# Optimization experiments

Hardware: AMD Instinct MI355X
Metric: run time of the kernel (lower is better)

Reference implementation:

```python
import jax, jax.numpy as jnp
import numpy as np

B, S, D, H, E = 2, 2048, 1024, 16, 8
DH = D // H
CAP_FACTOR = 1.2


def setup_inputs() -> dict:
    key = jax.random.key(0)
    ks = jax.random.split(key, 14)
    s = 0.02
    return {
        "embed": jax.random.normal(ks[0], (B, S, D), jnp.float32),
        "Wq": jax.random.normal(ks[1], (H, DH, D), jnp.float32) * s,
        "bq": jnp.zeros((H, DH), jnp.float32),
        "Wk": jax.random.normal(ks[2], (H, DH, D), jnp.float32) * s,
        "bk": jnp.zeros((H, DH), jnp.float32),
        "Wv": jax.random.normal(ks[3], (H, DH, D), jnp.float32) * s,
        "bv": jnp.zeros((H, DH), jnp.float32),
        "We": jax.random.normal(ks[4], (E, D, D), jnp.float32) * s,
        "be": jnp.zeros((E, D), jnp.float32),
        "Wsw": jax.random.normal(ks[5], (E, D), jnp.float32) * s,
        "bsw": jnp.zeros((E,), jnp.float32),
        "gamma": jnp.ones((D,), jnp.float32),
        "beta": jnp.zeros((D,), jnp.float32),
    }


def _forward(embed, Wq, bq, Wk, bk, Wv, bv, We, be, Wsw, bsw, gamma, beta):
    b, s, d = embed.shape
    h, e = Wq.shape[0], We.shape[0]
    # --- multi-head attention (all heads batched via einsum) ---
    q = jnp.einsum('bsd,hed->bhse', embed, Wq) + bq[None, :, None, :]
    k = jnp.einsum('bsd,hed->bhse', embed, Wk) + bk[None, :, None, :]
    v = jnp.einsum('bsd,hed->bhse', embed, Wv) + bv[None, :, None, :]
    att = jnp.einsum('bhse,bhte->bhst', q, k)  # [b,h,s,s]
    tril = jnp.tril(jnp.ones((s, s), bool))
    # faithful: upper triangle zeroed (NOT -inf), scale by sqrt(embedding_dim)
    att = jnp.where(tril, att, 0.0) / jnp.sqrt(jnp.float32(d))
    att = jax.nn.softmax(att, axis=-1)
    out = jnp.einsum('bhst,bhte->bhse', att, v)
    hiddens = out.transpose(0, 2, 1, 3).reshape(b, s, d)
    # --- SwitchLinear: top-1 token-choice routing with capacity drop ---
    x = hiddens.reshape(-1, d)  # [N, d]
    n = b * s
    capacity = int(CAP_FACTOR * n / e)
    logits = x @ Wsw.T + bsw
    probs = jax.nn.softmax(logits, axis=-1)
    route_probs = jnp.max(probs, axis=-1)
    routes = jnp.argmax(probs, axis=-1)
    onehot = jax.nn.one_hot(routes, e, dtype=jnp.int32)
    pos = jnp.cumsum(onehot, axis=0) - 1  # position within chosen expert
    pos = jnp.take_along_axis(pos, routes[:, None], axis=1)[:, 0]
    kept = pos < capacity
    slot = jnp.where(kept, routes * capacity + pos, e * capacity)  # overflow row
    dispatch = jnp.zeros((e * capacity + 1, d), x.dtype).at[slot].set(x)
    expert_in = dispatch[: e * capacity].reshape(e, capacity, d)
    expert_out = jnp.einsum('ecd,efd->ecf', expert_in, We) + be[:, None, :]
    expert_flat = jnp.concatenate(
        [expert_out.reshape(e * capacity, d), jnp.zeros((1, d), x.dtype)], 0)
    gathered = expert_flat[slot]
    y = jnp.where(kept[:, None], gathered, x)  # dropped tokens pass through
    y = (y * route_probs[:, None]).reshape(b, s, d)
    # --- residual + LayerNorm ---
    x2 = y + embed
    mean = jnp.mean(x2, axis=-1, keepdims=True)
    var = jnp.var(x2, axis=-1, keepdims=True)
    return (x2 - mean) / jnp.sqrt(var + 1e-5) * gamma + beta


def reference(embed, Wq, bq, Wk, bk, Wv, bv, We, be, Wsw, bsw, gamma, beta):
    return _forward(embed, Wq, bq, Wk, bk, Wv, bv, We, be, Wsw, bsw, gamma, beta)
```

## Files before the change

### kernel.cpp

```cpp
#include <hip/hip_runtime.h>

constexpr int B = 2, S = 2048, D = 1024, H = 16, E = 8, DH = 64;
constexpr int N = B * S;
constexpr int CAP = 614;
constexpr int ECAP = 640;
constexpr float INV_SQRT_D = 0.03125f;
constexpr int ATTN_LDS = 133120;

typedef __bf16 bf16x8 __attribute__((ext_vector_type(8)));
typedef float f32x4 __attribute__((ext_vector_type(4)));

__device__ __forceinline__ ushort f2bf(float x) {
  __bf16 h = (__bf16)x;
  return __builtin_bit_cast(unsigned short, h);
}
__device__ __forceinline__ float bf2f(ushort u) {
  __bf16 h = __builtin_bit_cast(__bf16, u);
  return (float)h;
}
__device__ __forceinline__ void gld16(const void* g, void* l) {
  __builtin_amdgcn_global_load_lds(
      (const __attribute__((address_space(1))) unsigned int*)g,
      (__attribute__((address_space(3))) unsigned int*)l, 16, 0, 0);
}

__global__ __launch_bounds__(256) void cvt_pair(const float* __restrict__ in,
                                                ushort* __restrict__ out)
{
  const long long idx4 = (long long)blockIdx.x * 256 + threadIdx.x;
  const float4 xv = ((const float4*)in)[idx4];
  const long long row = idx4 >> 8;
  const int col = (int)((idx4 & 255) << 2);
  float xs[4] = {xv.x, xv.y, xv.z, xv.w};
  ushort4 hi, lo;
  ushort* hp = (ushort*)&hi; ushort* lp = (ushort*)&lo;
  #pragma unroll
  for (int c = 0; c < 4; ++c) {
    ushort h = f2bf(xs[c]);
    hp[c] = h;
    lp[c] = f2bf(xs[c] - bf2f(h));
  }
  *(ushort4*)&out[row * 2048 + col] = hi;
  *(ushort4*)&out[row * 2048 + 1024 + col] = lo;
}

__global__ __launch_bounds__(256) void cvt_plain(const float* __restrict__ in,
                                                 ushort* __restrict__ out)
{
  const long long idx4 = (long long)blockIdx.x * 256 + threadIdx.x;
  const float4 xv = ((const float4*)in)[idx4];
  ushort4 o;
  o.x = f2bf(xv.x); o.y = f2bf(xv.y); o.z = f2bf(xv.z); o.w = f2bf(xv.w);
  *(ushort4*)&out[idx4 * 4] = o;
}

template <bool TRIPLE, int EPI>
__global__ __launch_bounds__(256) void mfma_gemm(
    const ushort* __restrict__ A, const ushort* __restrict__ W,
    const float* __restrict__ b0, const float* __restrict__ b1,
    const float* __restrict__ b2, float* __restrict__ C,
    ushort* __restrict__ pairout,
    long long strideA, long long strideW, long long strideC,
    long long biasStride, int biasSel)
{
  constexpr int KA = TRIPLE ? 2048 : 1024;
  constexpr int KW = TRIPLE ? 2048 : 1024;
  constexpr int NSTEP = TRIPLE ? 48 : 16;
  const int z = blockIdx.z;
  A += (long long)z * strideA;
  W += (long long)z * strideW;
  C += (long long)z * strideC;
  const float* bp = biasSel ? (z == 0 ? b0 : (z == 1 ? b1 : b2))
                            : b0 + (long long)z * biasStride;

  __shared__ char smem[32768] __attribute__((aligned(128)));
  const int tid = threadIdx.x;
  const int lane = tid & 63;
  const int lrow = lane & 15;
  const int lk = lane >> 4;
  const int wv = tid >> 6;
  const int rAc = (wv >> 1) * 64;
  const int rBc = (wv & 1) * 64;
  const int bm0 = blockIdx.y * 128;
  const int bn0 = blockIdx.x * 128;
  const int srow = tid >> 3;
  const int su = tid & 7;

  f32x4 acc[4][4] = {};

  for (int step = 0; step < NSTEP; ++step) {
    const int k0 = step * 64;
    int srcA, srcB;
    if (TRIPLE) {
      srcA = (k0 < 2048) ? k0 : k0 - 2048;
      srcB = (k0 < 1024) ? k0 : k0 - 1024;
    } else { srcA = k0; srcB = k0; }
    __syncthreads();
    #pragma unroll
    for (int i = 0; i < 4; ++i) {
      const int row = i * 32 + srow;
      const int u = su ^ (row & 7);
      gld16(A + (long long)(bm0 + row) * KA + srcA + u * 8,
            smem + i * 4096 + wv * 1024);
      gld16(W + (long long)(bn0 + row) * KW + srcB + u * 8,
            smem + 16384 + i * 4096 + wv * 1024);
    }
    asm volatile("s_waitcnt vmcnt(0)" ::: "memory");
    __syncthreads();
    #pragma unroll
    for (int h = 0; h < 2; ++h) {
      bf16x8 af[4], bfr[4];
      #pragma unroll
      for (int i = 0; i < 4; ++i) {
        const int row = rAc + i * 16 + lrow;
        const int u = (h * 4 + lk) ^ (row & 7);
        af[i] = *(const bf16x8*)(smem + row * 128 + u * 16);
      }
      #pragma unroll
      for (int j = 0; j < 4; ++j) {
        const int row = rBc + j * 16 + lrow;
        const int u = (h * 4 + lk) ^ (row & 7);
        bfr[j] = *(const bf16x8*)(smem + 16384 + row * 128 + u * 16);
      }
      #pragma unroll
      for (int i = 0; i < 4; ++i)
        #pragma unroll
        for (int j = 0; j < 4; ++j)
          acc[i][j] = __builtin_amdgcn_mfma_f32_16x16x32_bf16(
              af[i], bfr[j], acc[i][j], 0, 0, 0);
    }
  }
  const int rg = (lane >> 4) * 4;
  #pragma unroll
  for (int j = 0; j < 4; ++j) {
    const int col = bn0 + rBc + j * 16 + (lane & 15);
    const float bj = bp[col];
    #pragma unroll
    for (int i = 0; i < 4; ++i) {
      const int rbase = bm0 + rAc + i * 16 + rg;
      if constexpr (EPI == 0) {
        #pragma unroll
        for (int r = 0; r < 4; ++r)
          C[(long long)(rbase + r) * 1024 + col] = acc[i][j][r] + bj;
      } else {
        const int hh = col >> 6, e = col & 63;
        const int b = rbase >> 11;
        if (z < 2) {
          const int sbase = rbase & 2047;
          ushort* dst = pairout + (long long)z * 8388608 +
                        ((long long)(b * 16 + hh) * 2048 + sbase) * 128 + e;
          #pragma unroll
          for (int r = 0; r < 4; ++r) {
            float val = acc[i][j][r] + bj;
            ushort vh = f2bf(val);
            dst[r * 128] = vh;
            dst[r * 128 + 64] = f2bf(val - bf2f(vh));
          }
        } else {
          const int tb = rbase & 2047;
          ushort4 hi4, lo4;
          ushort* hp = (ushort*)&hi4; ushort* lp = (ushort*)&lo4;
          #pragma unroll
          for (int r = 0; r < 4; ++r) {
            float val = acc[i][j][r] + bj;
            ushort vh = f2bf(val);
            hp[r] = vh;
            lp[r] = f2bf(val - bf2f(vh));
          }
          ushort* vdst = pairout + 2ll * 8388608 +
                         (long long)(b * 16 + hh) * 262144 +
                         (long long)e * 2048 + tb;
          *(ushort4*)vdst = hi4;
          *(ushort4*)(vdst + 131072) = lo4;
        }
      }
    }
  }
}

__global__ __launch_bounds__(256) void suffix_kernel(const ushort* __restrict__ vtp,
                                                     float* __restrict__ vsuf)
{
  const int R = blockIdx.x;
  const int bh = R >> 6, e = R & 63;
  const ushort* hi = vtp + (long long)bh * 262144 + (long long)e * 2048;
  const ushort* lo = hi + 131072;
  const int tid = threadIdx.x;
  ushort4 h0 = *(const ushort4*)(hi + tid * 8);
  ushort4 h1 = *(const ushort4*)(hi + tid * 8 + 4);
  ushort4 l0 = *(const ushort4*)(lo + tid * 8);
  ushort4 l1 = *(const ushort4*)(lo + tid * 8 + 4);
  float v[8];
  v[0] = bf2f(h0.x) + bf2f(l0.x); v[1] = bf2f(h0.y) + bf2f(l0.y);
  v[2] = bf2f(h0.z) + bf2f(l0.z); v[3] = bf2f(h0.w) + bf2f(l0.w);
  v[4] = bf2f(h1.x) + bf2f(l1.x); v[5] = bf2f(h1.y) + bf2f(l1.y);
  v[6] = bf2f(h1.z) + bf2f(l1.z); v[7] = bf2f(h1.w) + bf2f(l1.w);
  float s = 0.f;
  #pragma unroll
  for (int x = 0; x < 8; ++x) s += v[x];
  __shared__ float ss[256];
  ss[tid] = s;
  __syncthreads();
  for (int off = 1; off < 256; off <<= 1) {
    float t = (tid + off < 256) ? ss[tid + off] : 0.f;
    __syncthreads();
    ss[tid] += t;
    __syncthreads();
  }
  float acc = (tid < 255) ? ss[tid + 1] : 0.f;
  float out[8];
  for (int x = 7; x >= 0; --x) { acc += v[x]; out[x] = acc; }
  #pragma unroll
  for (int x = 0; x < 8; ++x)
    vsuf[(long long)R * 2048 + tid * 8 + x] = out[x];
}

__device__ __forceinline__ void attn_stage_kv(
    const ushort* kbase, const ushort* vbase, int t0,
    char* kdst, char* vdst, int tid, int wv)
{
  #pragma unroll
  for (int i = 0; i < 2; ++i) {
    const int L = i * 512 + tid;
    const int row = L >> 4, u = L & 15;
    gld16(kbase + (long long)(t0 + row) * 128 + ((u ^ (row & 15)) * 8),
          kdst + i * 8192 + wv * 1024);
  }
  #pragma unroll
  for (int i = 0; i < 2; ++i) {
    const int L = i * 512 + tid;
    const int sec = L >> 9, vr = (L >> 3) & 63, u = L & 7;
    gld16(vbase + (long long)sec * 131072 + (long long)vr * 2048 + t0 +
              ((u ^ (vr & 7)) * 8),
          vdst + i * 8192 + wv * 1024);
  }
}

__global__ __launch_bounds__(512) void attn_mfma(
    const ushort* __restrict__ qp, const ushort* __restrict__ kp,
    const ushort* __restrict__ vtp, const float* __restrict__ vsuf,
    float* __restrict__ hid)
{
  extern __shared__ char smem[];
  const int bh = blockIdx.y;
  const int qi = (int)(gridDim.x - 1 - blockIdx.x);
  const int sB0 = qi * 128;
  const int tid = threadIdx.x;
  const int lane = tid & 63;
  const int wv = tid >> 6;
  const int g = lane >> 4, c = lane & 15;

  ushort* qs = (ushort*)smem;
  char* kbuf0 = smem + 32768;
  char* kbuf1 = smem + 49152;
  char* vbuf0 = smem + 65536;
  char* vbuf1 = smem + 81920;
  float* wl = (float*)(smem + 98304);

  const ushort* qbase = qp + (long long)bh * 2048 * 128;
  const ushort* kbase = kp + (long long)bh * 2048 * 128;
  const ushort* vbase = vtp + (long long)bh * 262144;

  #pragma unroll
  for (int i = 0; i < 4; ++i) {
    const int L = i * 512 + tid;
    const int row = L >> 4, u = L & 15;
    gld16(qbase + (long long)(sB0 + row) * 128 + ((u ^ (row & 15)) * 8),
          smem + i * 8192 + wv * 1024);
  }
  char* kcur = kbuf0; char* knext = kbuf1;
  char* vcur = vbuf0; char* vnext = vbuf1;
  attn_stage_kv(kbase, vbase, 0, kcur, vcur, tid, wv);

  f32x4 oacc[4] = {};
  float l_acc[4] = {};
  const int nt = 2 * qi + 2;
  const int qrow = wv * 16 + c;

  for (int t = 0; t < nt; ++t) {
    const int t0 = t * 64;
    if (t + 1 < nt) {
      attn_stage_kv(kbase, vbase, t0 + 64, knext, vnext, tid, wv);
      asm volatile("s_waitcnt vmcnt(4)" ::: "memory");
    } else {
      asm volatile("s_waitcnt vmcnt(0)" ::: "memory");
    }
    __builtin_amdgcn_s_barrier();

    const ushort* ks = (const ushort*)kcur;
    const ushort* vt = (const ushort*)vcur;

    f32x4 acc[4] = {};
    #pragma unroll
    for (int h = 0; h < 2; ++h) {
      bf16x8 qh = *(const bf16x8*)(qs + qrow * 128 + (((h * 4 + g) ^ (qrow & 15)) * 8));
      bf16x8 ql = *(const bf16x8*)(qs + qrow * 128 + (((8 + h * 4 + g) ^ (qrow & 15)) * 8));
      #pragma unroll
      for (int j = 0; j < 4; ++j) {
        const int krow = j * 16 + c;
        bf16x8 kh = *(const bf16x8*)(ks + krow * 128 + (((h * 4 + g) ^ (krow & 15)) * 8));
        bf16x8 kl = *(const bf16x8*)(ks + krow * 128 + (((8 + h * 4 + g) ^ (krow & 15)) * 8));
        acc[j] = __builtin_amdgcn_mfma_f32_16x16x32_bf16(qh, kh, acc[j], 0, 0, 0);
        acc[j] = __builtin_amdgcn_mfma_f32_16x16x32_bf16(ql, kh, acc[j], 0, 0, 0);
        acc[j] = __builtin_amdgcn_mfma_f32_16x16x32_bf16(qh, kl, acc[j], 0, 0, 0);
      }
    }

    float prt[4] = {0.f, 0.f, 0.f, 0.f};
    #pragma unroll
    for (int j = 0; j < 4; ++j) {
      #pragma unroll
      for (int r = 0; r < 4; ++r) {
        const int sg = sB0 + wv * 16 + 4 * g + r;
        const int tg = t0 + j * 16 + c;
        const float w = (tg <= sg) ? __expf(acc[j][r] * INV_SQRT_D) : 0.f;
        wl[(wv * 16 + 4 * g + r) * 68 + j * 16 + c] = w;
        prt[r] += w;
      }
    }
    #pragma unroll
    for (int off = 1; off < 16; off <<= 1)
      #pragma unroll
      for (int r = 0; r < 4; ++r) prt[r] += __shfl_xor(prt[r], off);
    #pragma unroll
    for (int r = 0; r < 4; ++r) l_acc[r] += prt[r];

    asm volatile("s_waitcnt lgkmcnt(0)" ::: "memory");
    __builtin_amdgcn_s_barrier();

    #pragma unroll
    for (int h = 0; h < 2; ++h) {
      const int wrow = wv * 16 + c;
      const float4 w0 = *(const float4*)&wl[wrow * 68 + h * 32 + g * 8];
      const float4 w1 = *(const float4*)&wl[wrow * 68 + h * 32 + g * 8 + 4];
      const float wf[8] = {w0.x, w0.y, w0.z, w0.w, w1.x, w1.y, w1.z, w1.w};
      bf16x8 wh, wlo;
      #pragma unroll
      for (int x = 0; x < 8; ++x) {
        __bf16 hh = (__bf16)wf[x];
        wh[x] = hh;
        wlo[x] = (__bf16)(wf[x] - (float)hh);
      }
      #pragma unroll
      for (int j = 0; j < 4; ++j) {
        const int vrow = j * 16 + c;
        bf16x8 vh = *(const bf16x8*)(vt + vrow * 64 + (((h * 4 + g) ^ (vrow & 7)) * 8));
        bf16x8 vl = *(const bf16x8*)(vt + 4096 + vrow * 64 + (((h * 4 + g) ^ (vrow & 7)) * 8));
        oacc[j] = __builtin_amdgcn_mfma_f32_16x16x32_bf16(wh, vh, oacc[j], 0, 0, 0);
        oacc[j] = __builtin_amdgcn_mfma_f32_16x16x32_bf16(wlo, vh, oacc[j], 0, 0, 0);
        oacc[j] = __builtin_amdgcn_mfma_f32_16x16x32_bf16(wh, vl, oacc[j], 0, 0, 0);
      }
    }
    __builtin_amdgcn_s_barrier();
    char* tk = kcur; kcur = knext; knext = tk;
    char* tv = vcur; vcur = vnext; vnext = tv;
  }

  const int b = bh >> 4, hh = bh & 15;
  #pragma unroll
  for (int r = 0; r < 4; ++r) {
    const int sg = sB0 + wv * 16 + 4 * g + r;
    const float denom = l_acc[r] + (float)(S - 1 - sg);
    #pragma unroll
    for (int j = 0; j < 4; ++j) {
      const int e = j * 16 + c;
      const float suf = (sg + 1 < S) ? vsuf[((long long)bh * 64 + e) * 2048 + sg + 1] : 0.f;
      hid[(long long)(b * S + sg) * 1024 + hh * 64 + e] = (oacc[j][r] + suf) / denom;
    }
  }
}

__global__ __launch_bounds__(256) void router_kernel(
    const float* __restrict__ x, const float* __restrict__ Wsw,
    const float* __restrict__ bsw, int* __restrict__ routes,
    float* __restrict__ rprob)
{
  const int w = threadIdx.x >> 6, lane = threadIdx.x & 63;
  const int i = blockIdx.x * 4 + w;
  float p[E] = {};
  const float4* xr = (const float4*)(x + (long long)i * D);
  #pragma unroll
  for (int t = 0; t < 4; ++t) {
    float4 xv = xr[lane + 64 * t];
    #pragma unroll
    for (int e = 0; e < E; ++e) {
      float4 wv = ((const float4*)(Wsw + e * D))[lane + 64 * t];
      p[e] += xv.x * wv.x + xv.y * wv.y + xv.z * wv.z + xv.w * wv.w;
    }
  }
  #pragma unroll
  for (int off = 32; off; off >>= 1)
    #pragma unroll
    for (int e = 0; e < E; ++e) p[e] += __shfl_xor(p[e], off);
  if (lane == 0) {
    float m = -1e30f; int arg = 0;
    #pragma unroll
    for (int e = 0; e < E; ++e) {
      float l = p[e] + bsw[e];
      if (l > m) { m = l; arg = e; }
      p[e] = l;
    }
    float sum = 0.f;
    #pragma unroll
    for (int e = 0; e < E; ++e) sum += __expf(p[e] - m);
    routes[i] = arg;
    rprob[i] = 1.f / sum;
  }
}

__global__ __launch_bounds__(256) void scan_kernel(const int* __restrict__ routes,
                                                   int* __restrict__ slot)
{
  __shared__ int hist[256][E];
  const int tid = threadIdx.x;
  const int per = N / 256;
  int cnt[E] = {};
  for (int j = 0; j < per; ++j) cnt[routes[tid * per + j]]++;
  #pragma unroll
  for (int e = 0; e < E; ++e) hist[tid][e] = cnt[e];
  __syncthreads();
  if (tid < E) {
    int run = 0;
    for (int t = 0; t < 256; ++t) { int tmp = hist[t][tid]; hist[t][tid] = run; run += tmp; }
  }
  __syncthreads();
  int run[E];
  #pragma unroll
  for (int e = 0; e < E; ++e) run[e] = hist[tid][e];
  for (int j = 0; j < per; ++j) {
    int i = tid * per + j;
    int r = routes[i];
    int pos = run[r]++;
    slot[i] = (pos < CAP) ? r * ECAP + pos : -1;
  }
}

__global__ __launch_bounds__(256) void dispatch_kernel(
    const float* __restrict__ x, const int* __restrict__ slot,
    ushort* __restrict__ expert_in)
{
  const int i = blockIdx.x;
  const int sl = slot[i];
  if (sl < 0) return;
  float4 xv = ((const float4*)&x[(long long)i * D])[threadIdx.x];
  ushort4 o;
  o.x = f2bf(xv.x); o.y = f2bf(xv.y); o.z = f2bf(xv.z); o.w = f2bf(xv.w);
  ((ushort4*)&expert_in[(long long)sl * D])[threadIdx.x] = o;
}

__global__ __launch_bounds__(256) void finalize_kernel(
    const float* __restrict__ x, const float* __restrict__ eout,
    const int* __restrict__ slot, const float* __restrict__ rprob,
    const float* __restrict__ embed, const float* __restrict__ gamma,
    const float* __restrict__ beta, float* __restrict__ out)
{
  const int i = blockIdx.x;
  const int tid = threadIdx.x;
  const int sl = slot[i];
  const float rp = rprob[i];
  const float4* src = (sl >= 0) ? (const float4*)&eout[(long long)sl * D]
                                : (const float4*)&x[(long long)i * D];
  float4 yv = src[tid];
  float4 ev = ((const float4*)&embed[(long long)i * D])[tid];
  float v0 = yv.x * rp + ev.x;
  float v1 = yv.y * rp + ev.y;
  float v2 = yv.z * rp + ev.z;
  float v3 = yv.w * rp + ev.w;
  float s1 = v0 + v1 + v2 + v3;
  float s2 = v0*v0 + v1*v1 + v2*v2 + v3*v3;
  #pragma unroll
  for (int off = 32; off; off >>= 1) {
    s1 += __shfl_xor(s1, off);
    s2 += __shfl_xor(s2, off);
  }
  __shared__ float wsum[4], wsq[4];
  const int wid = tid >> 6, lid = tid & 63;
  if (lid == 0) { wsum[wid] = s1; wsq[wid] = s2; }
  __syncthreads();
  float tot  = wsum[0] + wsum[1] + wsum[2] + wsum[3];
  float tot2 = wsq[0] + wsq[1] + wsq[2] + wsq[3];
  const float mean = tot * (1.f / D);
  const float var = tot2 * (1.f / D) - mean * mean;
  const float rstd = rsqrtf(var + 1e-5f);
  float4 gv = ((const float4*)gamma)[tid];
  float4 bv = ((const float4*)beta)[tid];
  float4 ov;
  ov.x = (v0 - mean) * rstd * gv.x + bv.x;
  ov.y = (v1 - mean) * rstd * gv.y + bv.y;
  ov.z = (v2 - mean) * rstd * gv.z + bv.z;
  ov.w = (v3 - mean) * rstd * gv.w + bv.w;
  ((float4*)&out[(long long)i * D])[tid] = ov;
}

extern "C" void kernel_launch(void* const* d_in, const int* in_sizes, int n_in,
                              void* d_out, int out_size, void* d_ws, size_t ws_size,
                              hipStream_t stream) {
  const float* embed = (const float*)d_in[0];
  const float* Wq = (const float*)d_in[1];
  const float* bq = (const float*)d_in[2];
  const float* Wk = (const float*)d_in[3];
  const float* bk = (const float*)d_in[4];
  const float* Wv = (const float*)d_in[5];
  const float* bv = (const float*)d_in[6];
  const float* We = (const float*)d_in[7];
  const float* be = (const float*)d_in[8];
  const float* Wsw = (const float*)d_in[9];
  const float* bsw = (const float*)d_in[10];
  const float* gamma = (const float*)d_in[11];
  const float* beta = (const float*)d_in[12];
  float* out = (float*)d_out;

  (void)hipFuncSetAttribute((const void*)attn_mfma,
                            hipFuncAttributeMaxDynamicSharedMemorySize,
                            ATTN_LDS);

  char* base = (char*)d_ws;
  ushort* epair      = (ushort*)base;
  float*  hid        = (float*)base;
  ushort* wpair      = (ushort*)(base + 16777216);
  ushort* expert_in  = (ushort*)(base + 16777216);
  ushort* pairs      = (ushort*)(base + 29360128);
  float*  expert_out = (float*)(base + 29360128);
  ushort* qp  = pairs;
  ushort* kp  = pairs + 8388608;
  ushort* vtp = pairs + 2 * 8388608;
  float*  vsuf = (float*)(base + 79691776);
  ushort* webf = (ushort*)(base + 79691776);
  int*    routes = (int*)(base + 96468992);
  int*    slot   = routes + N;
  float*  rprob  = (float*)(slot + N);

  cvt_pair<<<N * D / 1024, 256, 0, stream>>>(embed, epair);
  cvt_pair<<<D * D / 1024, 256, 0, stream>>>(Wq, wpair + 0ll * D * 2048);
  cvt_pair<<<D * D / 1024, 256, 0, stream>>>(Wk, wpair + 1ll * D * 2048);
  cvt_pair<<<D * D / 1024, 256, 0, stream>>>(Wv, wpair + 2ll * D * 2048);
  mfma_gemm<true, 1><<<dim3(8, 32, 3), 256, 0, stream>>>(
      epair, wpair, bq, bk, bv, nullptr, pairs,
      0, (long long)D * 2048, 0, 0, 1);
  suffix_kernel<<<B * H * 64, 256, 0, stream>>>(vtp, vsuf);
  attn_mfma<<<dim3(S / 128, B * H), 512, ATTN_LDS, stream>>>(
      qp, kp, vtp, vsuf, hid);
  router_kernel<<<N / 4, 256, 0, stream>>>(hid, Wsw, bsw, routes, rprob);
  scan_kernel<<<1, 256, 0, stream>>>(routes, slot);
  cvt_plain<<<(int)((long long)E * D * D / 1024), 256, 0, stream>>>(We, webf);
  dispatch_kernel<<<N, 256, 0, stream>>>(hid, slot, expert_in);
  mfma_gemm<false, 0><<<dim3(8, ECAP / 128, E), 256, 0, stream>>>(
      expert_in, webf, be, nullptr, nullptr, expert_out, nullptr,
      (long long)ECAP * D, (long long)D * D, (long long)ECAP * D,
      (long long)D, 0);
  finalize_kernel<<<N, 256, 0, stream>>>(hid, expert_out, slot, rprob,
                                         embed, gamma, beta, out);
}
```

Before: 469.3 us.

## Keep attention probabilities in registers and swizzle block order for QKV GEMM

```diff
diff --git a/kernel.cpp b/kernel.cpp
--- a/kernel.cpp
+++ b/kernel.cpp
@@ -5,10 +5,10 @@
 constexpr int CAP = 614;
 constexpr int ECAP = 640;
 constexpr float INV_SQRT_D = 0.03125f;
-constexpr int ATTN_LDS = 133120;
 
 typedef __bf16 bf16x8 __attribute__((ext_vector_type(8)));
 typedef float f32x4 __attribute__((ext_vector_type(4)));
+typedef unsigned int u32x4 __attribute__((ext_vector_type(4)));
 
 __device__ __forceinline__ ushort f2bf(float x) {
   __bf16 h = (__bf16)x;
@@ -54,26 +54,124 @@
   *(ushort4*)&out[idx4 * 4] = o;
 }
 
-template <bool TRIPLE, int EPI>
-__global__ __launch_bounds__(256) void mfma_gemm(
+__global__ __launch_bounds__(256) void qkv_gemm(
+    const ushort* __restrict__ A, const ushort* __restrict__ Wp,
+    const float* __restrict__ bq, const float* __restrict__ bk,
+    const float* __restrict__ bv, ushort* __restrict__ pairout)
+{
+  __shared__ char smem[32768] __attribute__((aligned(128)));
+  const int tid = threadIdx.x;
+  const int lane = tid & 63;
+  const int lrow = lane & 15;
+  const int lk = lane >> 4;
+  const int wv = tid >> 6;
+  const int rAc = (wv >> 1) * 64;
+  const int rBc = (wv & 1) * 64;
+  const int flat = (int)(blockIdx.y * 24 + blockIdx.x);
+  const int swz = (flat & 7) * 96 + (flat >> 3);
+  const int bn0 = (swz % 24) * 128;
+  const int bm0 = (swz / 24) * 128;
+  const int z = bn0 >> 10;
+  const ushort* Wt = Wp + (long long)z * (1024 * 2048) +
+                     (long long)(bn0 & 1023) * 2048;
+  const float* bp = (z == 0) ? bq : (z == 1) ? bk : bv;
+  const int srow = tid >> 3;
+  const int su = tid & 7;
+
+  f32x4 acc[4][4] = {};
+
+  for (int step = 0; step < 48; ++step) {
+    const int k0 = step * 64;
+    const int srcA = (k0 < 2048) ? k0 : k0 - 2048;
+    const int srcB = (k0 < 1024) ? k0 : k0 - 1024;
+    __syncthreads();
+    #pragma unroll
+    for (int i = 0; i < 4; ++i) {
+      const int row = i * 32 + srow;
+      const int u = su ^ (row & 7);
+      gld16(A + (long long)(bm0 + row) * 2048 + srcA + u * 8,
+            smem + i * 4096 + wv * 1024);
+      gld16(Wt + (long long)row * 2048 + srcB + u * 8,
+            smem + 16384 + i * 4096 + wv * 1024);
+    }
+    asm volatile("s_waitcnt vmcnt(0)" ::: "memory");
+    __syncthreads();
+    #pragma unroll
+    for (int h = 0; h < 2; ++h) {
+      bf16x8 af[4], bfr[4];
+      #pragma unroll
+      for (int i = 0; i < 4; ++i) {
+        const int row = rAc + i * 16 + lrow;
+        const int u = (h * 4 + lk) ^ (row & 7);
+        af[i] = *(const bf16x8*)(smem + row * 128 + u * 16);
+      }
+      #pragma unroll
+      for (int j = 0; j < 4; ++j) {
+        const int row = rBc + j * 16 + lrow;
+        const int u = (h * 4 + lk) ^ (row & 7);
+        bfr[j] = *(const bf16x8*)(smem + 16384 + row * 128 + u * 16);
+      }
+      #pragma unroll
+      for (int i = 0; i < 4; ++i)
+        #pragma unroll
+        for (int j = 0; j < 4; ++j)
+          acc[i][j] = __builtin_amdgcn_mfma_f32_16x16x32_bf16(
+              af[i], bfr[j], acc[i][j], 0, 0, 0);
+    }
+  }
+  const int rg = lk * 4;
+  #pragma unroll
+  for (int j = 0; j < 4; ++j) {
+    const int col = bn0 + rBc + j * 16 + lrow;
+    const int cz = col & 1023;
+    const float bj = bp[cz];
+    const int hh = cz >> 6, e = cz & 63;
+    #pragma unroll
+    for (int i = 0; i < 4; ++i) {
+      const int rbase = bm0 + rAc + i * 16 + rg;
+      const int b = rbase >> 11;
+      if (z < 2) {
+        const int sbase = rbase & 2047;
+        ushort* dst = pairout + (long long)z * 8388608 +
+                      ((long long)(b * 16 + hh) * 2048 + sbase) * 128 + e;
+        #pragma unroll
+        for (int r = 0; r < 4; ++r) {
+          float val = acc[i][j][r] + bj;
+          ushort vh = f2bf(val);
+          dst[r * 128] = vh;
+          dst[r * 128 + 64] = f2bf(val - bf2f(vh));
+        }
+      } else {
+        const int tb = rbase & 2047;
+        ushort4 hi4, lo4;
+        ushort* hp = (ushort*)&hi4; ushort* lp = (ushort*)&lo4;
+        #pragma unroll
+        for (int r = 0; r < 4; ++r) {
+          float val = acc[i][j][r] + bj;
+          ushort vh = f2bf(val);
+          hp[r] = vh;
+          lp[r] = f2bf(val - bf2f(vh));
+        }
+        ushort* vdst = pairout + 2ll * 8388608 +
+                       (long long)(b * 16 + hh) * 262144 +
+                       (long long)e * 2048 + tb;
+        *(ushort4*)vdst = hi4;
+        *(ushort4*)(vdst + 131072) = lo4;
+      }
+    }
+  }
+}
+
+__global__ __launch_bounds__(256) void expert_gemm(
     const ushort* __restrict__ A, const ushort* __restrict__ W,
-    const float* __restrict__ b0, const float* __restrict__ b1,
-    const float* __restrict__ b2, float* __restrict__ C,
-    ushort* __restrict__ pairout,
-    long long strideA, long long strideW, long long strideC,
-    long long biasStride, int biasSel)
-{
-  constexpr int KA = TRIPLE ? 2048 : 1024;
-  constexpr int KW = TRIPLE ? 2048 : 1024;
-  constexpr int NSTEP = TRIPLE ? 48 : 16;
+    const float* __restrict__ be, float* __restrict__ C)
+{
+  __shared__ char smem[32768] __attribute__((aligned(128)));
   const int z = blockIdx.z;
-  A += (long long)z * strideA;
-  W += (long long)z * strideW;
-  C += (long long)z * strideC;
-  const float* bp = biasSel ? (z == 0 ? b0 : (z == 1 ? b1 : b2))
-                            : b0 + (long long)z * biasStride;
-
-  __shared__ char smem[32768] __attribute__((aligned(128)));
+  A += (long long)z * (ECAP * D);
+  W += (long long)z * (D * D);
+  C += (long long)z * (ECAP * D);
+  const float* bp = be + (long long)z * D;
   const int tid = threadIdx.x;
   const int lane = tid & 63;
   const int lrow = lane & 15;
@@ -87,22 +185,16 @@
   const int su = tid & 7;
 
   f32x4 acc[4][4] = {};
-
-  for (int step = 0; step < NSTEP; ++step) {
+  for (int step = 0; step < 16; ++step) {
     const int k0 = step * 64;
-    int srcA, srcB;
-    if (TRIPLE) {
-      srcA = (k0 < 2048) ? k0 : k0 - 2048;
-      srcB = (k0 < 1024) ? k0 : k0 - 1024;
-    } else { srcA = k0; srcB = k0; }
     __syncthreads();
     #pragma unroll
     for (int i = 0; i < 4; ++i) {
       const int row = i * 32 + srow;
       const int u = su ^ (row & 7);
-      gld16(A + (long long)(bm0 + row) * KA + srcA + u * 8,
+      gld16(A + (long long)(bm0 + row) * 1024 + k0 + u * 8,
             smem + i * 4096 + wv * 1024);
-      gld16(W + (long long)(bn0 + row) * KW + srcB + u * 8,
+      gld16(W + (long long)(bn0 + row) * 1024 + k0 + u * 8,
             smem + 16384 + i * 4096 + wv * 1024);
     }
     asm volatile("s_waitcnt vmcnt(0)" ::: "memory");
@@ -130,50 +222,17 @@
               af[i], bfr[j], acc[i][j], 0, 0, 0);
     }
   }
-  const int rg = (lane >> 4) * 4;
+  const int rg = lk * 4;
   #pragma unroll
   for (int j = 0; j < 4; ++j) {
-    const int col = bn0 + rBc + j * 16 + (lane & 15);
+    const int col = bn0 + rBc + j * 16 + lrow;
     const float bj = bp[col];
     #pragma unroll
     for (int i = 0; i < 4; ++i) {
       const int rbase = bm0 + rAc + i * 16 + rg;
-      if constexpr (EPI == 0) {
-        #pragma unroll
-        for (int r = 0; r < 4; ++r)
-          C[(long long)(rbase + r) * 1024 + col] = acc[i][j][r] + bj;
-      } else {
-        const int hh = col >> 6, e = col & 63;
-        const int b = rbase >> 11;
-        if (z < 2) {
-          const int sbase = rbase & 2047;
-          ushort* dst = pairout + (long long)z * 8388608 +
-                        ((long long)(b * 16 + hh) * 2048 + sbase) * 128 + e;
-          #pragma unroll
-          for (int r = 0; r < 4; ++r) {
-            float val = acc[i][j][r] + bj;
-            ushort vh = f2bf(val);
-            dst[r * 128] = vh;
-            dst[r * 128 + 64] = f2bf(val - bf2f(vh));
-          }
-        } else {
-          const int tb = rbase & 2047;
-          ushort4 hi4, lo4;
-          ushort* hp = (ushort*)&hi4; ushort* lp = (ushort*)&lo4;
-          #pragma unroll
-          for (int r = 0; r < 4; ++r) {
-            float val = acc[i][j][r] + bj;
-            ushort vh = f2bf(val);
-            hp[r] = vh;
-            lp[r] = f2bf(val - bf2f(vh));
-          }
-          ushort* vdst = pairout + 2ll * 8388608 +
-                         (long long)(b * 16 + hh) * 262144 +
-                         (long long)e * 2048 + tb;
-          *(ushort4*)vdst = hi4;
-          *(ushort4*)(vdst + 131072) = lo4;
-        }
-      }
+      #pragma unroll
+      for (int r = 0; r < 4; ++r)
+        C[(long long)(rbase + r) * 1024 + col] = acc[i][j][r] + bj;
     }
   }
 }
@@ -236,29 +295,26 @@
   }
 }
 
-__global__ __launch_bounds__(512) void attn_mfma(
+__global__ __launch_bounds__(512, 4) void attn_mfma(
     const ushort* __restrict__ qp, const ushort* __restrict__ kp,
     const ushort* __restrict__ vtp, const float* __restrict__ vsuf,
     float* __restrict__ hid)
 {
-  extern __shared__ char smem[];
-  const int bh = blockIdx.y;
-  const int qi = (int)(gridDim.x - 1 - blockIdx.x);
-  const int sB0 = qi * 128;
+  __shared__ char smem[65536] __attribute__((aligned(128)));
   const int tid = threadIdx.x;
   const int lane = tid & 63;
   const int wv = tid >> 6;
   const int g = lane >> 4, c = lane & 15;
 
-  ushort* qs = (ushort*)smem;
-  char* kbuf0 = smem + 32768;
-  char* kbuf1 = smem + 49152;
-  char* vbuf0 = smem + 65536;
-  char* vbuf1 = smem + 81920;
-  float* wl = (float*)(smem + 98304);
-
-  const ushort* qbase = qp + (long long)bh * 2048 * 128;
-  const ushort* kbase = kp + (long long)bh * 2048 * 128;
+  const int flat = (int)(blockIdx.y * 16 + blockIdx.x);
+  const int swz = (flat & 7) * 64 + (flat >> 3);
+  const int bh = swz >> 4;
+  const int bx = swz & 15;
+  const int qi = ((bh >> 1) & 1) ? (15 - bx) : bx;
+  const int sB0 = qi * 128;
+
+  const ushort* qbase = qp + (long long)bh * (2048 * 128);
+  const ushort* kbase = kp + (long long)bh * (2048 * 128);
   const ushort* vbase = vtp + (long long)bh * 262144;
 
   #pragma unroll
@@ -268,19 +324,38 @@
     gld16(qbase + (long long)(sB0 + row) * 128 + ((u ^ (row & 15)) * 8),
           smem + i * 8192 + wv * 1024);
   }
-  char* kcur = kbuf0; char* knext = kbuf1;
-  char* vcur = vbuf0; char* vnext = vbuf1;
-  attn_stage_kv(kbase, vbase, 0, kcur, vcur, tid, wv);
+  asm volatile("s_waitcnt vmcnt(0)" ::: "memory");
+  __builtin_amdgcn_s_barrier();
+  bf16x8 qh[2], ql[2];
+  {
+    const int qrow = wv * 16 + c;
+    const ushort* qsl = (const ushort*)smem + qrow * 128;
+    #pragma unroll
+    for (int h = 0; h < 2; ++h) {
+      qh[h] = *(const bf16x8*)(qsl + (((h * 4 + g) ^ c) * 8));
+      ql[h] = *(const bf16x8*)(qsl + (((8 + h * 4 + g) ^ c) * 8));
+    }
+  }
+  asm volatile("s_waitcnt lgkmcnt(0)" ::: "memory");
+  __builtin_amdgcn_s_barrier();
+
+  attn_stage_kv(kbase, vbase, 0, smem, smem + 32768, tid, wv);
 
   f32x4 oacc[4] = {};
-  float l_acc[4] = {};
+  float l_acc = 0.f;
   const int nt = 2 * qi + 2;
-  const int qrow = wv * 16 + c;
+  const int srcA = ((lane >> 4) & 1) * 32 + c;
+  const int srcB = srcA + 16;
+  const bool ghi = lane >= 32;
 
   for (int t = 0; t < nt; ++t) {
     const int t0 = t * 64;
+    char* kcur = smem + (t & 1) * 16384;
+    char* vcur = smem + 32768 + (t & 1) * 16384;
     if (t + 1 < nt) {
-      attn_stage_kv(kbase, vbase, t0 + 64, knext, vnext, tid, wv);
+      attn_stage_kv(kbase, vbase, t0 + 64,
+                    smem + ((t + 1) & 1) * 16384,
+                    smem + 32768 + ((t + 1) & 1) * 16384, tid, wv);
       asm volatile("s_waitcnt vmcnt(4)" ::: "memory");
     } else {
       asm volatile("s_waitcnt vmcnt(0)" ::: "memory");
@@ -291,76 +366,89 @@
     const ushort* vt = (const ushort*)vcur;
 
     f32x4 acc[4] = {};
+    __builtin_amdgcn_s_setprio(1);
     #pragma unroll
     for (int h = 0; h < 2; ++h) {
-      bf16x8 qh = *(const bf16x8*)(qs + qrow * 128 + (((h * 4 + g) ^ (qrow & 15)) * 8));
-      bf16x8 ql = *(const bf16x8*)(qs + qrow * 128 + (((8 + h * 4 + g) ^ (qrow & 15)) * 8));
       #pragma unroll
       for (int j = 0; j < 4; ++j) {
         const int krow = j * 16 + c;
-        bf16x8 kh = *(const bf16x8*)(ks + krow * 128 + (((h * 4 + g) ^ (krow & 15)) * 8));
-        bf16x8 kl = *(const bf16x8*)(ks + krow * 128 + (((8 + h * 4 + g) ^ (krow & 15)) * 8));
-        acc[j] = __builtin_amdgcn_mfma_f32_16x16x32_bf16(qh, kh, acc[j], 0, 0, 0);
-        acc[j] = __builtin_amdgcn_mfma_f32_16x16x32_bf16(ql, kh, acc[j], 0, 0, 0);
-        acc[j] = __builtin_amdgcn_mfma_f32_16x16x32_bf16(qh, kl, acc[j], 0, 0, 0);
-      }
-    }
-
-    float prt[4] = {0.f, 0.f, 0.f, 0.f};
-    #pragma unroll
-    for (int j = 0; j < 4; ++j) {
+        const ushort* kr = ks + krow * 128;
+        bf16x8 kh = *(const bf16x8*)(kr + (((h * 4 + g) ^ c) * 8));
+        bf16x8 kl = *(const bf16x8*)(kr + (((8 + h * 4 + g) ^ c) * 8));
+        acc[j] = __builtin_amdgcn_mfma_f32_16x16x32_bf16(kh, qh[h], acc[j], 0, 0, 0);
+        acc[j] = __builtin_amdgcn_mfma_f32_16x16x32_bf16(kl, qh[h], acc[j], 0, 0, 0);
+        acc[j] = __builtin_amdgcn_mfma_f32_16x16x32_bf16(kh, ql[h], acc[j], 0, 0, 0);
+      }
+    }
+    __builtin_amdgcn_s_setprio(0);
+
+    unsigned int pw[16];
+    float prt = 0.f;
+    const int sg_c = sB0 + wv * 16 + c;
+    #pragma unroll
+    for (int j = 0; j < 4; ++j)
       #pragma unroll
       for (int r = 0; r < 4; ++r) {
-        const int sg = sB0 + wv * 16 + 4 * g + r;
-        const int tg = t0 + j * 16 + c;
-        const float w = (tg <= sg) ? __expf(acc[j][r] * INV_SQRT_D) : 0.f;
-        wl[(wv * 16 + 4 * g + r) * 68 + j * 16 + c] = w;
-        prt[r] += w;
-      }
-    }
-    #pragma unroll
-    for (int off = 1; off < 16; off <<= 1)
-      #pragma unroll
-      for (int r = 0; r < 4; ++r) prt[r] += __shfl_xor(prt[r], off);
-    #pragma unroll
-    for (int r = 0; r < 4; ++r) l_acc[r] += prt[r];
-
+        const int tg = t0 + j * 16 + 4 * g + r;
+        float w = (tg <= sg_c) ? __expf(acc[j][r] * INV_SQRT_D) : 0.f;
+        prt += w;
+        ushort hi = f2bf(w);
+        ushort lo = f2bf(w - bf2f(hi));
+        pw[j * 4 + r] = (unsigned)hi | ((unsigned)lo << 16);
+      }
+    prt += __shfl_xor(prt, 16);
+    prt += __shfl_xor(prt, 32);
+    l_acc += prt;
+
+    unsigned int paw[2][8];
+    #pragma unroll
+    for (int h = 0; h < 2; ++h)
+      #pragma unroll
+      for (int r = 0; r < 4; ++r) {
+        unsigned a0 = (unsigned)__shfl((int)pw[(2 * h) * 4 + r], srcA);
+        unsigned a1 = (unsigned)__shfl((int)pw[(2 * h + 1) * 4 + r], srcA);
+        unsigned b0 = (unsigned)__shfl((int)pw[(2 * h) * 4 + r], srcB);
+        unsigned b1 = (unsigned)__shfl((int)pw[(2 * h + 1) * 4 + r], srcB);
+        paw[h][r] = ghi ? a1 : a0;
+        paw[h][4 + r] = ghi ? b1 : b0;
+      }
+    bf16x8 pah[2], pal[2];
+    #pragma unroll
+    for (int h = 0; h < 2; ++h) {
+      u32x4 hv, lv;
+      #pragma unroll
+      for (int p = 0; p < 4; ++p) {
+        hv[p] = (paw[h][2 * p] & 0xffffu) | (paw[h][2 * p + 1] << 16);
+        lv[p] = (paw[h][2 * p] >> 16) | (paw[h][2 * p + 1] & 0xffff0000u);
+      }
+      pah[h] = __builtin_bit_cast(bf16x8, hv);
+      pal[h] = __builtin_bit_cast(bf16x8, lv);
+    }
+
+    __builtin_amdgcn_s_setprio(1);
+    #pragma unroll
+    for (int h = 0; h < 2; ++h)
+      #pragma unroll
+      for (int j = 0; j < 4; ++j) {
+        const int vrow = j * 16 + c;
+        const ushort* vr = vt + vrow * 64;
+        bf16x8 vh = *(const bf16x8*)(vr + (((h * 4 + g) ^ (c & 7)) * 8));
+        bf16x8 vl = *(const bf16x8*)(vr + 4096 + (((h * 4 + g) ^ (c & 7)) * 8));
+        oacc[j] = __builtin_amdgcn_mfma_f32_16x16x32_bf16(pah[h], vh, oacc[j], 0, 0, 0);
+        oacc[j] = __builtin_amdgcn_mfma_f32_16x16x32_bf16(pal[h], vh, oacc[j], 0, 0, 0);
+        oacc[j] = __builtin_amdgcn_mfma_f32_16x16x32_bf16(pah[h], vl, oacc[j], 0, 0, 0);
+      }
+    __builtin_amdgcn_s_setprio(0);
     asm volatile("s_waitcnt lgkmcnt(0)" ::: "memory");
     __builtin_amdgcn_s_barrier();
-
-    #pragma unroll
-    for (int h = 0; h < 2; ++h) {
-      const int wrow = wv * 16 + c;
-      const float4 w0 = *(const float4*)&wl[wrow * 68 + h * 32 + g * 8];
-      const float4 w1 = *(const float4*)&wl[wrow * 68 + h * 32 + g * 8 + 4];
-      const float wf[8] = {w0.x, w0.y, w0.z, w0.w, w1.x, w1.y, w1.z, w1.w};
-      bf16x8 wh, wlo;
-      #pragma unroll
-      for (int x = 0; x < 8; ++x) {
-        __bf16 hh = (__bf16)wf[x];
-        wh[x] = hh;
-        wlo[x] = (__bf16)(wf[x] - (float)hh);
-      }
-      #pragma unroll
-      for (int j = 0; j < 4; ++j) {
-        const int vrow = j * 16 + c;
-        bf16x8 vh = *(const bf16x8*)(vt + vrow * 64 + (((h * 4 + g) ^ (vrow & 7)) * 8));
-        bf16x8 vl = *(const bf16x8*)(vt + 4096 + vrow * 64 + (((h * 4 + g) ^ (vrow & 7)) * 8));
-        oacc[j] = __builtin_amdgcn_mfma_f32_16x16x32_bf16(wh, vh, oacc[j], 0, 0, 0);
-        oacc[j] = __builtin_amdgcn_mfma_f32_16x16x32_bf16(wlo, vh, oacc[j], 0, 0, 0);
-        oacc[j] = __builtin_amdgcn_mfma_f32_16x16x32_bf16(wh, vl, oacc[j], 0, 0, 0);
-      }
-    }
-    __builtin_amdgcn_s_barrier();
-    char* tk = kcur; kcur = knext; knext = tk;
-    char* tv = vcur; vcur = vnext; vnext = tv;
   }
 
   const int b = bh >> 4, hh = bh & 15;
   #pragma unroll
   for (int r = 0; r < 4; ++r) {
+    const float lr = __shfl(l_acc, (lane & 48) | (4 * g + r));
     const int sg = sB0 + wv * 16 + 4 * g + r;
-    const float denom = l_acc[r] + (float)(S - 1 - sg);
+    const float denom = lr + (float)(S - 1 - sg);
     #pragma unroll
     for (int j = 0; j < 4; ++j) {
       const int e = j * 16 + c;
@@ -510,10 +598,6 @@
   const float* beta = (const float*)d_in[12];
   float* out = (float*)d_out;
 
-  (void)hipFuncSetAttribute((const void*)attn_mfma,
-                            hipFuncAttributeMaxDynamicSharedMemorySize,
-                            ATTN_LDS);
-
   char* base = (char*)d_ws;
   ushort* epair      = (ushort*)base;
   float*  hid        = (float*)base;
@@ -534,20 +618,15 @@
   cvt_pair<<<D * D / 1024, 256, 0, stream>>>(Wq, wpair + 0ll * D * 2048);
   cvt_pair<<<D * D / 1024, 256, 0, stream>>>(Wk, wpair + 1ll * D * 2048);
   cvt_pair<<<D * D / 1024, 256, 0, stream>>>(Wv, wpair + 2ll * D * 2048);
-  mfma_gemm<true, 1><<<dim3(8, 32, 3), 256, 0, stream>>>(
-      epair, wpair, bq, bk, bv, nullptr, pairs,
-      0, (long long)D * 2048, 0, 0, 1);
+  qkv_gemm<<<dim3(24, 32), 256, 0, stream>>>(epair, wpair, bq, bk, bv, pairs);
   suffix_kernel<<<B * H * 64, 256, 0, stream>>>(vtp, vsuf);
-  attn_mfma<<<dim3(S / 128, B * H), 512, ATTN_LDS, stream>>>(
-      qp, kp, vtp, vsuf, hid);
+  attn_mfma<<<dim3(16, 32), 512, 0, stream>>>(qp, kp, vtp, vsuf, hid);
   router_kernel<<<N / 4, 256, 0, stream>>>(hid, Wsw, bsw, routes, rprob);
   scan_kernel<<<1, 256, 0, stream>>>(routes, slot);
   cvt_plain<<<(int)((long long)E * D * D / 1024), 256, 0, stream>>>(We, webf);
   dispatch_kernel<<<N, 256, 0, stream>>>(hid, slot, expert_in);
-  mfma_gemm<false, 0><<<dim3(8, ECAP / 128, E), 256, 0, stream>>>(
-      expert_in, webf, be, nullptr, nullptr, expert_out, nullptr,
-      (long long)ECAP * D, (long long)D * D, (long long)ECAP * D,
-      (long long)D, 0);
+  expert_gemm<<<dim3(8, ECAP / 128, E), 256, 0, stream>>>(
+      expert_in, webf, be, expert_out);
   finalize_kernel<<<N, 256, 0, stream>>>(hid, expert_out, slot, rprob,
                                          embed, gamma, beta, out);
 }
```

Result: faster. 404.7 us (-13.8%).
